# Kernel optimization log

Hardware: AMD Instinct MI355X
Metric: run time of the kernel (lower is better)

Reference implementation:

```python
import jax, jax.numpy as jnp
import numpy as np

ALPHA = 0.5
NOISE_KEY = jax.random.key(42)  # fixed key: deterministic stand-in for torch.randn


def setup_inputs() -> dict:
    key = jax.random.key(0)
    k1, k2 = jax.random.split(key)
    N, D, E = 8192, 1024, 131072
    x = jax.random.normal(k1, (N, D), dtype=jnp.float32)
    edge_index = jax.random.randint(k2, (2, E), 0, N, dtype=jnp.int64)
    return {"x": x, "edge_index": edge_index}


def reference(x, edge_index):
    # edge_index is accepted but unused, matching the original module.
    N = x.shape[0]
    m = jax.random.normal(NOISE_KEY, (N, N), dtype=x.dtype)  # [N, N] noise
    M = jax.nn.softmax(m / ALPHA, axis=1)                    # row-wise Gibbs weights
    return M @ x                                             # [N, D]
```

## Files before the change

kernel.cpp:

```cpp
#include <hip/hip_runtime.h>
#include <stdint.h>
#include <stddef.h>

#define NROWS 8192
#define NCOLS 8192
#define DDIM  1024

typedef float  f32x4 __attribute__((ext_vector_type(4)));
typedef _Float16 f16x8 __attribute__((ext_vector_type(8)));

#if __has_builtin(__builtin_amdgcn_exp2f)
#define EXP2F(x) __builtin_amdgcn_exp2f(x)
#else
#define EXP2F(x) exp2f(x)
#endif
#if __has_builtin(__builtin_amdgcn_logf)
#define LOG2F(x) __builtin_amdgcn_logf(x)
#else
#define LOG2F(x) log2f(x)
#endif
#if __has_builtin(__builtin_amdgcn_sqrtf)
#define SQRTF(x) __builtin_amdgcn_sqrtf(x)
#else
#define SQRTF(x) sqrtf(x)
#endif

__device__ __forceinline__ uint32_t rotl32(uint32_t x, uint32_t r){
  return (x << r) | (x >> (32u - r));
}

__device__ __forceinline__ void threefry2x32(uint32_t x0, uint32_t x1,
                                             uint32_t& o0, uint32_t& o1){
  const uint32_t k0 = 0u, k1 = 42u;
  const uint32_t k2 = k0 ^ k1 ^ 0x1BD11BDAu;
  x0 += k0; x1 += k1;
#define TF_R(r) { x0 += x1; x1 = rotl32(x1, r); x1 ^= x0; }
  TF_R(13) TF_R(15) TF_R(26) TF_R(6)
  x0 += k1; x1 += k2 + 1u;
  TF_R(17) TF_R(29) TF_R(16) TF_R(24)
  x0 += k2; x1 += k0 + 2u;
  TF_R(13) TF_R(15) TF_R(26) TF_R(6)
  x0 += k0; x1 += k1 + 3u;
  TF_R(17) TF_R(29) TF_R(16) TF_R(24)
  x0 += k1; x1 += k2 + 4u;
  TF_R(13) TF_R(15) TF_R(26) TF_R(6)
  x0 += k2; x1 += k0 + 5u;
#undef TF_R
  o0 = x0; o1 = x1;
}

__device__ __forceinline__ float elemE(uint32_t f){
  uint32_t o0, o1;
  threefry2x32(0u, f, o0, o1);
  const uint32_t b = o0 ^ o1;
  float u = __uint_as_float((b >> 9) | 0x3F800000u) - 1.0f;
  const float lo = -0.99999994f;
  float v = fmaf(u, 2.0f, lo);
  v = fmaxf(v, lo);
  const float t1 = fmaf(-v, v, 1.0f);
  float w = LOG2F(t1) * (-0.69314718f);
  float p;
  if (w < 5.0f){
    w -= 2.5f;
    p =              3.97426473e-08f;
    p = fmaf(p, w,   4.85465e-07f);
    p = fmaf(p, w,  -4.98283e-06f);
    p = fmaf(p, w,  -6.21053e-06f);
    p = fmaf(p, w,   3.09120e-04f);
    p = fmaf(p, w,  -1.77290e-03f);
    p = fmaf(p, w,  -5.90817e-03f);
    p = fmaf(p, w,   3.48803163e-01f);
    p = fmaf(p, w,   2.12331355e+00f);
  } else {
    w = SQRTF(w) - 3.0f;
    p =             -2.83147363e-04f;
    p = fmaf(p, w,   1.42765560e-04f);
    p = fmaf(p, w,   1.90825981e-03f);
    p = fmaf(p, w,  -5.19500608e-03f);
    p = fmaf(p, w,   8.11688602e-03f);
    p = fmaf(p, w,  -1.07798386e-02f);
    p = fmaf(p, w,   1.33487061e-02f);
    p = fmaf(p, w,   1.41658096e+00f);
    p = fmaf(p, w,   4.00643396e+00f);
  }
  const float m = p * v;
  return EXP2F(fmaf(m, 2.8853900817779268f, -4.0f));
}

__device__ __forceinline__ uint16_t f2h(float a){
  union { _Float16 h; uint16_t u; } c; c.h = (_Float16)a; return c.u;
}

__global__ __launch_bounds__(256) void transpose_cast(const float* __restrict__ x,
                                                      uint16_t* __restrict__ xT){
  __shared__ float tile[32][33];
  const int tx = threadIdx.x & 31;
  const int ty = threadIdx.x >> 5;
  const int dcol = blockIdx.x * 32;
  const int nrow = blockIdx.y * 32;
  #pragma unroll
  for (int r = 0; r < 32; r += 8)
    tile[ty + r][tx] = x[(size_t)(nrow + ty + r) * DDIM + dcol + tx];
  __syncthreads();
  #pragma unroll
  for (int r = 0; r < 32; r += 8)
    xT[(size_t)(dcol + ty + r) * NROWS + nrow + tx] = f2h(tile[tx][ty + r]);
}

__global__ __launch_bounds__(256) void gen_rows(uint16_t* __restrict__ P,
                                                float* __restrict__ S, int row0){
  const int gi = row0 + blockIdx.x;
  const uint32_t base = (uint32_t)gi * 8192u;
  const int t = threadIdx.x;
  uint16_t* __restrict__ prow = P + (size_t)blockIdx.x * NCOLS;
  float acc = 0.0f;
  #pragma unroll
  for (int g = 0; g < 4; ++g){
    const uint32_t j0 = (uint32_t)(g * 2048) + ((uint32_t)t << 3);
    float e[8];
    #pragma unroll
    for (int i = 0; i < 8; ++i){
      e[i] = elemE(base + j0 + (uint32_t)i);
      acc += e[i];
    }
    f16x8 pk;
    #pragma unroll
    for (int i = 0; i < 8; ++i) pk[i] = (_Float16)e[i];
    *reinterpret_cast<f16x8*>(prow + j0) = pk;
  }
  #pragma unroll
  for (int off = 32; off > 0; off >>= 1) acc += __shfl_down(acc, off, 64);
  __shared__ float sm[4];
  if ((t & 63) == 0) sm[t >> 6] = acc;
  __syncthreads();
  if (t == 0) S[gi] = (sm[0] + sm[1]) + (sm[2] + sm[3]);
}

#define BM 128
#define BN 128
#define BK 32

typedef const __attribute__((address_space(1))) void GAS;
typedef __attribute__((address_space(3))) void LAS;

__device__ __forceinline__ void gload16(const void* g, void* l){
  __builtin_amdgcn_global_load_lds((GAS*)g, (LAS*)l, 16, 0, 0);
}

__global__ __launch_bounds__(256, 2) void gemm_rows(
    const uint16_t* __restrict__ P,
    const uint16_t* __restrict__ xT,
    const float* __restrict__ S,
    int row0,
    float* __restrict__ O)
{
  __shared__ uint16_t smem[8192];
  uint16_t* As = smem;
  uint16_t* Bs = smem + 4096;

  const int tid  = threadIdx.x;
  const int lane = tid & 63;
  const int wave = tid >> 6;
  const int wr = (wave >> 1) * 64;
  const int wc = (wave & 1) * 64;
  const int l15 = lane & 15;
  const int lq  = lane >> 4;

  const size_t m0 = (size_t)blockIdx.x * BM;
  const size_t n0 = (size_t)blockIdx.y * BN;

  const int lin0 = tid, lin1 = tid + 256;
  const int r0s = lin0 >> 2, k0s = (lin0 & 3) << 3;
  const int r1s = lin1 >> 2, k1s = (lin1 & 3) << 3;

  const uint16_t* gA0 = P  + (m0 + r0s) * (size_t)NCOLS + k0s;
  const uint16_t* gA1 = P  + (m0 + r1s) * (size_t)NCOLS + k1s;
  const uint16_t* gB0 = xT + (n0 + r0s) * (size_t)NCOLS + k0s;
  const uint16_t* gB1 = xT + (n0 + r1s) * (size_t)NCOLS + k1s;

  f32x4 acc[4][4];
  #pragma unroll
  for (int i = 0; i < 4; ++i)
    #pragma unroll
    for (int j = 0; j < 4; ++j)
      #pragma unroll
      for (int q = 0; q < 4; ++q) acc[i][j][q] = 0.0f;

  for (int k0 = 0; k0 < NCOLS; k0 += BK){
    gload16(gA0 + k0, As + lin0 * 8);
    gload16(gA1 + k0, As + lin1 * 8);
    gload16(gB0 + k0, Bs + lin0 * 8);
    gload16(gB1 + k0, Bs + lin1 * 8);
    __syncthreads();
    f16x8 af[4], bfrag[4];
    #pragma unroll
    for (int i = 0; i < 4; ++i)
      af[i] = *reinterpret_cast<const f16x8*>(As + (wr + i*16 + l15) * BK + lq * 8);
    #pragma unroll
    for (int j = 0; j < 4; ++j)
      bfrag[j] = *reinterpret_cast<const f16x8*>(Bs + (wc + j*16 + l15) * BK + lq * 8);
    #pragma unroll
    for (int i = 0; i < 4; ++i)
      #pragma unroll
      for (int j = 0; j < 4; ++j)
        acc[i][j] = __builtin_amdgcn_mfma_f32_16x16x32_f16(af[i], bfrag[j], acc[i][j], 0, 0, 0);
    __syncthreads();
  }

  #pragma unroll
  for (int i = 0; i < 4; ++i){
    float rinv[4];
    #pragma unroll
    for (int r = 0; r < 4; ++r)
      rinv[r] = 1.0f / S[row0 + m0 + wr + i*16 + lq*4 + r];
    #pragma unroll
    for (int j = 0; j < 4; ++j){
      const size_t col = n0 + wc + j*16 + l15;
      #pragma unroll
      for (int r = 0; r < 4; ++r){
        const size_t row = m0 + wr + i*16 + lq*4 + r;
        O[row * DDIM + col] = acc[i][j][r] * rinv[r];
      }
    }
  }
}

extern "C" void kernel_launch(void* const* d_in, const int* in_sizes, int n_in,
                              void* d_out, int out_size, void* d_ws, size_t ws_size,
                              hipStream_t stream)
{
  (void)in_sizes; (void)n_in; (void)out_size;
  const float* x = (const float*)d_in[0];
  float* O = (float*)d_out;
  uint8_t* ws = (uint8_t*)d_ws;

  float* S = (float*)ws;
  const size_t S_bytes = (size_t)NROWS * sizeof(float);
  uint16_t* xT = (uint16_t*)(ws + S_bytes);
  const size_t xT_bytes = (size_t)DDIM * NROWS * sizeof(uint16_t);
  uint16_t* P = (uint16_t*)(ws + S_bytes + xT_bytes);
  const size_t used = S_bytes + xT_bytes;
  const size_t avail = ws_size > used ? ws_size - used : 0;

  transpose_cast<<<dim3(DDIM/32, NROWS/32), 256, 0, stream>>>(x, xT);

  const size_t fullP = (size_t)NROWS * NCOLS * sizeof(uint16_t);
  if (avail >= fullP){
    gen_rows<<<NROWS, 256, 0, stream>>>(P, S, 0);
    gemm_rows<<<dim3(NROWS/BM, DDIM/BN), 256, 0, stream>>>(P, xT, S, 0, O);
  } else {
    int R = 128;
    for (int r = 4096; r >= 128; r >>= 1)
      if ((size_t)r * NCOLS * sizeof(uint16_t) <= avail){ R = r; break; }
    for (int r0 = 0; r0 < NROWS; r0 += R){
      gen_rows<<<R, 256, 0, stream>>>(P, S, r0);
      gemm_rows<<<dim3(R/BM, DDIM/BN), 256, 0, stream>>>(P, xT, S, r0, O + (size_t)r0 * DDIM);
    }
  }
}
```

Baseline: 364.4 us.

## Fuse transpose into noise generation and double GEMM K-tile with XOR-swizzled LDS

The x transpose/cast is folded into the noise-generation kernel, with each of the 8192 blocks transposing one 32x32 tile before generating its row, which removes a separate launch. The GEMM K-tile grows from 32 to 64, so each barrier pair covers two MFMA k-steps. LDS chunk placement is XOR-swizzled to avoid bank conflicts on fragment reads. Occupancy is hinted at 3 blocks/CU despite doubled shared memory, which risks more register pressure or spills.

```diff
diff --git a/kernel.cpp b/kernel.cpp
--- a/kernel.cpp
+++ b/kernel.cpp
@@ -107,6 +107,49 @@
     xT[(size_t)(dcol + ty + r) * NROWS + nrow + tx] = f2h(tile[tx][ty + r]);
 }
 
+__global__ __launch_bounds__(256) void gen_trans_rows(const float* __restrict__ x,
+                                                      uint16_t* __restrict__ xT,
+                                                      uint16_t* __restrict__ P,
+                                                      float* __restrict__ S){
+  const int t = threadIdx.x;
+  {
+    __shared__ float tile[32][33];
+    const int tx = t & 31;
+    const int ty = t >> 5;
+    const int dcol = (blockIdx.x & 31) * 32;
+    const int nrow = (blockIdx.x >> 5) * 32;
+    #pragma unroll
+    for (int r = 0; r < 32; r += 8)
+      tile[ty + r][tx] = x[(size_t)(nrow + ty + r) * DDIM + dcol + tx];
+    __syncthreads();
+    #pragma unroll
+    for (int r = 0; r < 32; r += 8)
+      xT[(size_t)(dcol + ty + r) * NROWS + nrow + tx] = f2h(tile[tx][ty + r]);
+  }
+  const int gi = blockIdx.x;
+  const uint32_t base = (uint32_t)gi * 8192u;
+  uint16_t* __restrict__ prow = P + (size_t)gi * NCOLS;
+  float acc = 0.0f;
+  #pragma unroll
+  for (int g = 0; g < 4; ++g){
+    const uint32_t j0 = (uint32_t)(g * 2048) + ((uint32_t)t << 3);
+    float e[8];
+    #pragma unroll
+    for (int i = 0; i < 8; ++i){ e[i] = elemE(base + j0 + (uint32_t)i); acc += e[i]; }
+    f16x8 pk;
+    #pragma unroll
+    for (int i = 0; i < 8; ++i) pk[i] = (_Float16)e[i];
+    *reinterpret_cast<f16x8*>(prow + j0) = pk;
+  }
+  #pragma unroll
+  for (int off = 32; off > 0; off >>= 1) acc += __shfl_down(acc, off, 64);
+  __shared__ float sm[4];
+  __syncthreads();
+  if ((t & 63) == 0) sm[t >> 6] = acc;
+  __syncthreads();
+  if (t == 0) S[gi] = (sm[0] + sm[1]) + (sm[2] + sm[3]);
+}
+
 __global__ __launch_bounds__(256) void gen_rows(uint16_t* __restrict__ P,
                                                 float* __restrict__ S, int row0){
   const int gi = row0 + blockIdx.x;
@@ -119,10 +162,7 @@
     const uint32_t j0 = (uint32_t)(g * 2048) + ((uint32_t)t << 3);
     float e[8];
     #pragma unroll
-    for (int i = 0; i < 8; ++i){
-      e[i] = elemE(base + j0 + (uint32_t)i);
-      acc += e[i];
-    }
+    for (int i = 0; i < 8; ++i){ e[i] = elemE(base + j0 + (uint32_t)i); acc += e[i]; }
     f16x8 pk;
     #pragma unroll
     for (int i = 0; i < 8; ++i) pk[i] = (_Float16)e[i];
@@ -138,7 +178,7 @@
 
 #define BM 128
 #define BN 128
-#define BK 32
+#define BK 64
 
 typedef const __attribute__((address_space(1))) void GAS;
 typedef __attribute__((address_space(3))) void LAS;
@@ -147,16 +187,16 @@
   __builtin_amdgcn_global_load_lds((GAS*)g, (LAS*)l, 16, 0, 0);
 }
 
-__global__ __launch_bounds__(256, 2) void gemm_rows(
+__global__ __launch_bounds__(256, 3) void gemm_rows(
     const uint16_t* __restrict__ P,
     const uint16_t* __restrict__ xT,
     const float* __restrict__ S,
     int row0,
     float* __restrict__ O)
 {
-  __shared__ uint16_t smem[8192];
+  __shared__ uint16_t smem[16384];
   uint16_t* As = smem;
-  uint16_t* Bs = smem + 4096;
+  uint16_t* Bs = smem + 8192;
 
   const int tid  = threadIdx.x;
   const int lane = tid & 63;
@@ -169,14 +209,10 @@
   const size_t m0 = (size_t)blockIdx.x * BM;
   const size_t n0 = (size_t)blockIdx.y * BN;
 
-  const int lin0 = tid, lin1 = tid + 256;
-  const int r0s = lin0 >> 2, k0s = (lin0 & 3) << 3;
-  const int r1s = lin1 >> 2, k1s = (lin1 & 3) << 3;
-
-  const uint16_t* gA0 = P  + (m0 + r0s) * (size_t)NCOLS + k0s;
-  const uint16_t* gA1 = P  + (m0 + r1s) * (size_t)NCOLS + k1s;
-  const uint16_t* gB0 = xT + (n0 + r0s) * (size_t)NCOLS + k0s;
-  const uint16_t* gB1 = xT + (n0 + r1s) * (size_t)NCOLS + k1s;
+  const int srow = tid >> 3;
+  const int sx   = (tid & 7) ^ (srow & 7);
+  const uint16_t* gA = P  + (m0 + srow) * (size_t)NCOLS + sx * 8;
+  const uint16_t* gB = xT + (n0 + srow) * (size_t)NCOLS + sx * 8;
 
   f32x4 acc[4][4];
   #pragma unroll
@@ -186,24 +222,32 @@
       #pragma unroll
       for (int q = 0; q < 4; ++q) acc[i][j][q] = 0.0f;
 
+  const int axor = l15 & 7;
+
   for (int k0 = 0; k0 < NCOLS; k0 += BK){
-    gload16(gA0 + k0, As + lin0 * 8);
-    gload16(gA1 + k0, As + lin1 * 8);
-    gload16(gB0 + k0, Bs + lin0 * 8);
-    gload16(gB1 + k0, Bs + lin1 * 8);
+    #pragma unroll
+    for (int r = 0; r < 4; ++r)
+      gload16(gA + (size_t)(32 * r) * NCOLS + k0, As + (tid + 256 * r) * 8);
+    #pragma unroll
+    for (int r = 0; r < 4; ++r)
+      gload16(gB + (size_t)(32 * r) * NCOLS + k0, Bs + (tid + 256 * r) * 8);
     __syncthreads();
-    f16x8 af[4], bfrag[4];
-    #pragma unroll
-    for (int i = 0; i < 4; ++i)
-      af[i] = *reinterpret_cast<const f16x8*>(As + (wr + i*16 + l15) * BK + lq * 8);
-    #pragma unroll
-    for (int j = 0; j < 4; ++j)
-      bfrag[j] = *reinterpret_cast<const f16x8*>(Bs + (wc + j*16 + l15) * BK + lq * 8);
-    #pragma unroll
-    for (int i = 0; i < 4; ++i)
+    #pragma unroll
+    for (int ks = 0; ks < 2; ++ks){
+      const int kphys = ((lq + 4 * ks) ^ axor) * 8;
+      f16x8 af[4], bfrag[4];
+      #pragma unroll
+      for (int i = 0; i < 4; ++i)
+        af[i] = *reinterpret_cast<const f16x8*>(As + (wr + i*16 + l15) * BK + kphys);
       #pragma unroll
       for (int j = 0; j < 4; ++j)
-        acc[i][j] = __builtin_amdgcn_mfma_f32_16x16x32_f16(af[i], bfrag[j], acc[i][j], 0, 0, 0);
+        bfrag[j] = *reinterpret_cast<const f16x8*>(Bs + (wc + j*16 + l15) * BK + kphys);
+      #pragma unroll
+      for (int i = 0; i < 4; ++i)
+        #pragma unroll
+        for (int j = 0; j < 4; ++j)
+          acc[i][j] = __builtin_amdgcn_mfma_f32_16x16x32_f16(af[i], bfrag[j], acc[i][j], 0, 0, 0);
+    }
     __syncthreads();
   }
 
@@ -242,13 +286,12 @@
   const size_t used = S_bytes + xT_bytes;
   const size_t avail = ws_size > used ? ws_size - used : 0;
 
-  transpose_cast<<<dim3(DDIM/32, NROWS/32), 256, 0, stream>>>(x, xT);
-
   const size_t fullP = (size_t)NROWS * NCOLS * sizeof(uint16_t);
   if (avail >= fullP){
-    gen_rows<<<NROWS, 256, 0, stream>>>(P, S, 0);
+    gen_trans_rows<<<NROWS, 256, 0, stream>>>(x, xT, P, S);
     gemm_rows<<<dim3(NROWS/BM, DDIM/BN), 256, 0, stream>>>(P, xT, S, 0, O);
   } else {
+    transpose_cast<<<dim3(DDIM/32, NROWS/32), 256, 0, stream>>>(x, xT);
     int R = 128;
     for (int r = 4096; r >= 128; r >>= 1)
       if ((size_t)r * NCOLS * sizeof(uint16_t) <= avail){ R = r; break; }
```

New measurement: 327.7 us. 1.11x faster.
